# Performance work log

Measured on AMD Instinct MI355X. Metric: run time of the kernel, lower is better.

Reference implementation:

```python
import jax, jax.numpy as jnp
import numpy as np

DIM = 512      # model dim
HEADS = 8      # attention heads
WS = 256       # window_size
G = 32         # num_global_tokens
SPARSITY = 0.3 # fraction of entries masked out per row by the sparsity controller


def setup_inputs() -> dict:
    key = jax.random.key(0)
    ks = jax.random.split(key, 7)
    b, n = 4, 8192
    x = jax.random.normal(ks[0], (b, n, DIM), dtype=jnp.float32)
    w_qkv = jax.random.normal(ks[1], (DIM, 3 * DIM), dtype=jnp.float32) * (DIM ** -0.5)
    w_out = jax.random.normal(ks[2], (DIM, DIM), dtype=jnp.float32) * (DIM ** -0.5)
    b_out = jnp.zeros((DIM,), dtype=jnp.float32)
    local_bias = jax.random.normal(ks[3], (HEADS, WS, WS), dtype=jnp.float32)
    global_param = jax.random.normal(ks[4], (HEADS, G, WS), dtype=jnp.float32)
    gate = jax.random.normal(ks[5], (HEADS,), dtype=jnp.float32)
    return {"x": x, "w_qkv": w_qkv, "w_out": w_out, "b_out": b_out,
            "local_bias": local_bias, "global_param": global_param, "gate": gate}


def reference(x, w_qkv, w_out, b_out, local_bias, global_param, gate):
    b, n, _ = x.shape
    h, ws, g = HEADS, WS, G
    d = DIM // h
    w = n // ws  # number of windows
    scale = DIM ** -0.5

    qkv = x @ w_qkv                      # [b, n, 3*dim]
    q, k, v = jnp.split(qkv, 3, axis=-1)

    def to_win(t):  # [b, n, dim] -> [b, h, w, ws, d]
        return t.reshape(b, n, h, d).transpose(0, 2, 1, 3).reshape(b, h, w, ws, d)

    q, k, v = to_win(q), to_win(k), to_win(v)

    # windowed local attention with learned per-window additive bias
    local = jnp.einsum('bhwnd,bhwmd->bhwnm', q, k) * scale   # [b,h,w,ws,ws]
    local = local + local_bias[None, :, None]                # bias broadcast over b, w

    # global-token attention term built from window-averaged q/k
    q_mean = q.mean(axis=2)  # [b,h,ws,d]
    k_mean = k.mean(axis=2)  # [b,h,ws,d]
    global_q = jnp.einsum('hgn,bhnd->bhgd', global_param, q_mean)      # [b,h,g,d]
    global_scores = jnp.einsum('bhgd,bhmd->bhgm', global_q, k_mean) * scale  # [b,h,g,ws]
    global_bias = global_scores.mean(axis=2)                            # [b,h,ws]

    # sparsity controller: learned per-head gate combines local + global,
    # then top-k row sparsification keeps (1-sparsity) of entries pre-softmax
    gate_h = jax.nn.sigmoid(gate)[None, :, None, None, None]
    scores = local + gate_h * global_bias[:, :, None, None, :]          # [b,h,w,ws,ws]
    k_keep = int(ws * (1.0 - SPARSITY))
    thresh = jax.lax.top_k(scores, k_keep)[0][..., -1:]                 # kth largest per row
    scores = jnp.where(scores >= thresh, scores, jnp.float32(-1e9))

    attn = jax.nn.softmax(scores, axis=-1)
    out = jnp.einsum('bhwnm,bhwmd->bhwnd', attn, v)                     # [b,h,w,ws,d]
    out = out.reshape(b, h, n, d).transpose(0, 2, 1, 3).reshape(b, n, DIM)
    return out @ w_out + b_out
```

## Files before the change

### kernel.cpp

```cpp
#include <hip/hip_runtime.h>

#define NN    8192
#define WSZ   256
#define KKEEP 179
#define SCALE 0.044194173824159216f

typedef __attribute__((ext_vector_type(8))) __bf16 bf16x8;
typedef __attribute__((ext_vector_type(4))) short  s16x4;
typedef __attribute__((ext_vector_type(8))) short  s16x8;
typedef __attribute__((ext_vector_type(4))) float  f32x4;

struct Split3 { short h, m, l; };
__device__ __forceinline__ Split3 split3(float x)
{
    unsigned u  = __float_as_uint(x);
    unsigned hb = ((u + 0x7FFFu + ((u >> 16) & 1u)) >> 16) << 16;
    float r = x - __uint_as_float(hb);
    unsigned ur = __float_as_uint(r);
    unsigned mb = ((ur + 0x7FFFu + ((ur >> 16) & 1u)) >> 16) << 16;
    float r2 = r - __uint_as_float(mb);
    unsigned lr = __float_as_uint(r2);
    unsigned lb = (lr + 0x7FFFu + ((lr >> 16) & 1u)) >> 16;
    Split3 s;
    s.h = (short)(hb >> 16);
    s.m = (short)(mb >> 16);
    s.l = (short)(lb & 0xFFFFu);
    return s;
}

__device__ __forceinline__ void split2(float x, short& h, short& m)
{
    unsigned u  = __float_as_uint(x);
    unsigned hb = ((u + 0x7FFFu + ((u >> 16) & 1u)) >> 16) << 16;
    float r = x - __uint_as_float(hb);
    unsigned ur = __float_as_uint(r);
    unsigned mb = (ur + 0x7FFFu + ((ur >> 16) & 1u)) >> 16;
    h = (short)(hb >> 16);
    m = (short)(mb & 0xFFFFu);
}

__global__ __launch_bounds__(256) void splitw_kernel(const float* __restrict__ W,
                                                     int K, int N,
                                                     short* __restrict__ h,
                                                     short* __restrict__ m,
                                                     short* __restrict__ l)
{
    int idx = blockIdx.x * 256 + threadIdx.x;
    if (idx >= K * N) return;
    int k = idx / N, n = idx - k * N;
    Split3 s = split3(W[idx]);
    size_t o = (size_t)n * K + k;
    h[o] = s.h; m[o] = s.m; l[o] = s.l;
}

__global__ __launch_bounds__(256, 2) void gemm_mfma(const float* __restrict__ A, int lda,
                                                    const short* __restrict__ BTh,
                                                    const short* __restrict__ BTm,
                                                    const short* __restrict__ BTl,
                                                    const float* __restrict__ bias,
                                                    float* __restrict__ C, int ldc,
                                                    int qk_cols)
{
    __shared__ __align__(16) short Asm[3][128 * 40];
    __shared__ __align__(16) short Bsm[3][128 * 40];

    const int t       = threadIdx.x;
    const int lane    = t & 63;
    const int wave    = t >> 6;
    const int wr      = wave >> 1;
    const int wc      = wave & 1;
    const int rowBase = blockIdx.y * 128;
    const int colBase = blockIdx.x * 128;
    const int pstart  = (colBase < qk_cols) ? 0 : 3;

    const int sa[6] = {2, 0, 1, 1, 0, 0};
    const int sb[6] = {0, 2, 1, 0, 1, 0};

    const int fn = lane & 15;
    const int fq = (lane >> 4) * 8;

    f32x4 acc[4][4] = {};

    for (int ks = 0; ks < 512; ks += 32) {
        __syncthreads();

#pragma unroll
        for (int lo = 0; lo < 4; ++lo) {
            int idx = lo * 256 + t;
            int am  = idx >> 3;
            int af  = (idx & 7) * 4;
            float4 a4 = *(const float4*)&A[(size_t)(rowBase + am) * lda + ks + af];
            Split3 s0 = split3(a4.x);
            Split3 s1 = split3(a4.y);
            Split3 s2 = split3(a4.z);
            Split3 s3 = split3(a4.w);
            s16x4 hv, mv, lv;
            hv[0] = s0.h; hv[1] = s1.h; hv[2] = s2.h; hv[3] = s3.h;
            mv[0] = s0.m; mv[1] = s1.m; mv[2] = s2.m; mv[3] = s3.m;
            lv[0] = s0.l; lv[1] = s1.l; lv[2] = s2.l; lv[3] = s3.l;
            int o = am * 40 + af;
            *(s16x4*)&Asm[0][o] = hv;
            *(s16x4*)&Asm[1][o] = mv;
            *(s16x4*)&Asm[2][o] = lv;
        }
#pragma unroll
        for (int lo = 0; lo < 2; ++lo) {
            int c = lo * 256 + t;
            int n = c >> 2;
            int q = (c & 3) * 8;
            size_t src = (size_t)(colBase + n) * 512 + ks + q;
            int o = n * 40 + q;
            *(s16x8*)&Bsm[0][o] = *(const s16x8*)&BTh[src];
            *(s16x8*)&Bsm[1][o] = *(const s16x8*)&BTm[src];
            *(s16x8*)&Bsm[2][o] = *(const s16x8*)&BTl[src];
        }
        __syncthreads();

        bf16x8 Bf[3][4];
#pragma unroll
        for (int s = 0; s < 3; ++s)
#pragma unroll
            for (int j = 0; j < 4; ++j)
                Bf[s][j] = *(const bf16x8*)&Bsm[s][(wc * 64 + j * 16 + fn) * 40 + fq];

#pragma unroll
        for (int i = 0; i < 4; ++i) {
            bf16x8 Af[3];
#pragma unroll
            for (int s = 0; s < 3; ++s)
                Af[s] = *(const bf16x8*)&Asm[s][(wr * 64 + i * 16 + fn) * 40 + fq];
#pragma unroll
            for (int p = 0; p < 6; ++p) {
                if (p < pstart) continue;
#pragma unroll
                for (int j = 0; j < 4; ++j)
                    acc[i][j] = __builtin_amdgcn_mfma_f32_16x16x32_bf16(
                        Af[sa[p]], Bf[sb[p]][j], acc[i][j], 0, 0, 0);
            }
        }
    }

    const int crow0 = rowBase + wr * 64 + (lane >> 4) * 4;
    const int ccol0 = colBase + wc * 64 + fn;
#pragma unroll
    for (int j = 0; j < 4; ++j) {
        int col = ccol0 + j * 16;
        float bv = bias ? bias[col] : 0.0f;
#pragma unroll
        for (int i = 0; i < 4; ++i)
#pragma unroll
            for (int r = 0; r < 4; ++r)
                C[(size_t)(crow0 + i * 16 + r) * ldc + col] = acc[i][j][r] + bv;
    }
}

__global__ __launch_bounds__(256) void means_kernel(const float* __restrict__ qkv,
                                                    float* __restrict__ q_mean,
                                                    float* __restrict__ k_mean)
{
    int idx = blockIdx.x * 256 + threadIdx.x;
    int dd = idx & 63;
    int i  = (idx >> 6) & 255;
    int bh = idx >> 14;
    int b = bh >> 3, h = bh & 7;
    const float* base = qkv + (size_t)b * NN * 1536 + (size_t)h * 64 + dd;
    float qs = 0.f, ks = 0.f;
#pragma unroll
    for (int w = 0; w < 32; ++w) {
        size_t off = (size_t)(w * 256 + i) * 1536;
        qs += base[off];
        ks += base[off + 512];
    }
    q_mean[idx] = qs * 0.03125f;
    k_mean[idx] = ks * 0.03125f;
}

__global__ __launch_bounds__(256) void globalbias_kernel(const float* __restrict__ q_mean,
                                                         const float* __restrict__ k_mean,
                                                         const float* __restrict__ gp,
                                                         float* __restrict__ gbias)
{
    __shared__ float gq[32 * 64];
    const int bh = blockIdx.x;
    const int h  = bh & 7;
    const int t  = threadIdx.x;

#pragma unroll
    for (int e = 0; e < 8; ++e) {
        int idx = e * 256 + t;
        int g  = idx >> 6;
        int dd = idx & 63;
        const float* gpr = gp + (size_t)(h * 32 + g) * 256;
        const float* qm  = q_mean + (size_t)bh * 16384 + dd;
        float s = 0.f;
        for (int i = 0; i < 256; ++i) s += gpr[i] * qm[(size_t)i * 64];
        gq[idx] = s;
    }
    __syncthreads();

    const float* km = k_mean + (size_t)bh * 16384 + (size_t)t * 64;
    float4 kr[16];
#pragma unroll
    for (int j = 0; j < 16; ++j) kr[j] = *(const float4*)&km[4 * j];
    float acc = 0.f;
    for (int g = 0; g < 32; ++g) {
        const float* gqr = &gq[g * 64];
        float s = 0.f;
#pragma unroll
        for (int j = 0; j < 16; ++j) {
            float4 q4 = *(const float4*)&gqr[4 * j];
            s += q4.x * kr[j].x + q4.y * kr[j].y + q4.z * kr[j].z + q4.w * kr[j].w;
        }
        acc += s;
    }
    gbias[bh * 256 + t] = acc * SCALE * 0.03125f;
}

__device__ __forceinline__ unsigned mono_enc(float f) {
    unsigned u = __float_as_uint(f);
    return (u & 0x80000000u) ? ~u : (u | 0x80000000u);
}
__device__ __forceinline__ float mono_dec(unsigned e) {
    return (e & 0x80000000u) ? __uint_as_float(e ^ 0x80000000u)
                             : __uint_as_float(~e);
}

__global__ __launch_bounds__(256, 3) void attn_kernel(float* __restrict__ qkv,
                                                      const float* __restrict__ local_bias,
                                                      const float* __restrict__ gbias,
                                                      const float* __restrict__ gate)
{
    __shared__ __align__(16) short Qs[3 * 64 * 64];
    __shared__ __align__(16) short Ks[3 * 64 * 64];
    float* st = (float*)(void*)Ks;

    const int t    = threadIdx.x;
    const int lane = t & 63;
    const int wave = t >> 6;
    const int wr   = wave >> 1;
    const int wc   = wave & 1;
    const int fn   = lane & 15;
    const int fq   = (lane >> 4) * 8;
    const int g4   = (lane >> 4) * 4;

    const int blk = blockIdx.x;
    const int rc  = blk & 3;
    const int w   = (blk >> 2) & 31;
    const int bh  = blk >> 7;
    const int h   = bh & 7;
    const int b   = bh >> 3;
    const float gateh = 1.0f / (1.0f + __expf(-gate[h]));

    const size_t tokBase = (size_t)b * NN + (size_t)w * WSZ;
    float* qb = qkv + tokBase * 1536 + h * 64;
    const float* kb = qb + 512;
    const float* vb = qb + 1024;

    const int rr = t >> 2, sub = t & 3;

    const int sa[6] = {2, 0, 1, 1, 0, 0};
    const int sb[6] = {0, 2, 1, 0, 1, 0};

#pragma unroll
    for (int l = 0; l < 4; ++l) {
        int f  = l * 256 + t;
        int r  = f >> 4;
        int dg = (f & 15) * 4;
        float4 a4 = *(const float4*)&qb[(size_t)(rc * 64 + r) * 1536 + dg];
        Split3 s0 = split3(a4.x), s1 = split3(a4.y), s2 = split3(a4.z), s3 = split3(a4.w);
        s16x4 hv, mv, lv;
        hv[0] = s0.h; hv[1] = s1.h; hv[2] = s2.h; hv[3] = s3.h;
        mv[0] = s0.m; mv[1] = s1.m; mv[2] = s2.m; mv[3] = s3.m;
        lv[0] = s0.l; lv[1] = s1.l; lv[2] = s2.l; lv[3] = s3.l;
        int o = r * 64 + (dg ^ ((r & 7) << 3));
        *(s16x4*)&Qs[o]        = hv;
        *(s16x4*)&Qs[4096 + o] = mv;
        *(s16x4*)&Qs[8192 + o] = lv;
    }

    float vals[64];
#pragma unroll
    for (int mc = 0; mc < 4; ++mc) {
        __syncthreads();
#pragma unroll
        for (int l = 0; l < 4; ++l) {
            int f  = l * 256 + t;
            int m  = f >> 4;
            int dg = (f & 15) * 4;
            float4 a4 = *(const float4*)&kb[(size_t)(mc * 64 + m) * 1536 + dg];
            Split3 s0 = split3(a4.x), s1 = split3(a4.y), s2 = split3(a4.z), s3 = split3(a4.w);
            s16x4 hv, mv, lv;
            hv[0] = s0.h; hv[1] = s1.h; hv[2] = s2.h; hv[3] = s3.h;
            mv[0] = s0.m; mv[1] = s1.m; mv[2] = s2.m; mv[3] = s3.m;
            lv[0] = s0.l; lv[1] = s1.l; lv[2] = s2.l; lv[3] = s3.l;
            int o = m * 64 + (dg ^ ((m & 7) << 3));
            *(s16x4*)&Ks[o]        = hv;
            *(s16x4*)&Ks[4096 + o] = mv;
            *(s16x4*)&Ks[8192 + o] = lv;
        }
        __syncthreads();

        f32x4 acc[2][2] = {};
#pragma unroll
        for (int kk = 0; kk < 2; ++kk) {
            bf16x8 Af[3][2], Bf[3][2];
#pragma unroll
            for (int s = 0; s < 3; ++s)
#pragma unroll
                for (int i = 0; i < 2; ++i) {
                    int ar = wr * 32 + i * 16 + fn;
                    int bc = wc * 32 + i * 16 + fn;
                    Af[s][i] = *(const bf16x8*)&Qs[s * 4096 + ar * 64 + ((kk * 32 + fq) ^ ((ar & 7) << 3))];
                    Bf[s][i] = *(const bf16x8*)&Ks[s * 4096 + bc * 64 + ((kk * 32 + fq) ^ ((bc & 7) << 3))];
                }
#pragma unroll
            for (int p = 0; p < 6; ++p)
#pragma unroll
                for (int i = 0; i < 2; ++i)
#pragma unroll
                    for (int j = 0; j < 2; ++j)
                        acc[i][j] = __builtin_amdgcn_mfma_f32_16x16x32_bf16(
                            Af[sa[p]][i], Bf[sb[p]][j], acc[i][j], 0, 0, 0);
        }
        __syncthreads();

#pragma unroll
        for (int j = 0; j < 2; ++j) {
            int cl = wc * 32 + j * 16 + fn;
            int cf = mc * 64 + cl;
            float gb = gateh * gbias[bh * 256 + cf];
#pragma unroll
            for (int i = 0; i < 2; ++i)
#pragma unroll
                for (int r = 0; r < 4; ++r) {
                    int rl = wr * 32 + i * 16 + g4 + r;
                    st[rl * 68 + cl] = acc[i][j][r] * SCALE
                        + local_bias[((size_t)h * 256 + rc * 64 + rl) * 256 + cf] + gb;
                }
        }
        __syncthreads();
#pragma unroll
        for (int j = 0; j < 16; ++j)
            vals[mc * 16 + j] = st[rr * 68 + sub + 4 * j];
    }

    float rmin = vals[0], rmax = vals[0];
#pragma unroll
    for (int j = 1; j < 64; ++j) {
        rmin = fminf(rmin, vals[j]);
        rmax = fmaxf(rmax, vals[j]);
    }
    rmin = fminf(rmin, __shfl_xor(rmin, 1)); rmin = fminf(rmin, __shfl_xor(rmin, 2));
    rmax = fmaxf(rmax, __shfl_xor(rmax, 1)); rmax = fmaxf(rmax, __shfl_xor(rmax, 2));

    float flo = rmin, fhi = rmax;
    float thr = 0.f;
    bool  done = false;
    for (int it = 0; it < 16; ++it) {
        if (__all(done ? 1 : 0)) break;
        float mf = 0.5f * (flo + fhi);
        int c = 0;
#pragma unroll
        for (int j = 0; j < 64; ++j) c += (vals[j] >= mf) ? 1 : 0;
        c += __shfl_xor(c, 1);
        c += __shfl_xor(c, 2);
        if (!done) {
            if (c == KKEEP)      { thr = mf; done = true; }
            else if (c > KKEEP)  flo = mf;
            else                 fhi = mf;
        }
    }
    if (__any(done ? 0 : 1)) {
        unsigned lo_u = mono_enc(flo), hi_u = mono_enc(fhi);
        for (int it = 0; it < 34; ++it) {
            bool active = (!done) && (lo_u < hi_u);
            if (!__any(active ? 1 : 0)) break;
            unsigned span = hi_u - lo_u;
            unsigned mid  = lo_u + (span >> 1) + (span & 1u);
            float mf = mono_dec(mid);
            int c = 0;
#pragma unroll
            for (int j = 0; j < 64; ++j) c += (vals[j] >= mf) ? 1 : 0;
            c += __shfl_xor(c, 1);
            c += __shfl_xor(c, 2);
            if (active) {
                if (c == KKEEP)      { thr = mf; done = true; }
                else if (c >= KKEEP) lo_u = mid;
                else                 hi_u = mid - 1;
            }
        }
        if (!done) thr = mono_dec(lo_u);
    }

    float rmx = -3e38f;
#pragma unroll
    for (int j = 0; j < 64; ++j) rmx = fmaxf(rmx, (vals[j] >= thr) ? vals[j] : -3e38f);
    rmx = fmaxf(rmx, __shfl_xor(rmx, 1));
    rmx = fmaxf(rmx, __shfl_xor(rmx, 2));
    float rsum = 0.f;
#pragma unroll
    for (int j = 0; j < 64; ++j) {
        float e = (vals[j] >= thr) ? __expf(vals[j] - rmx) : 0.f;
        vals[j] = e;
        rsum += e;
    }
    rsum += __shfl_xor(rsum, 1);
    rsum += __shfl_xor(rsum, 2);
    float rinv = 1.0f / rsum;
#pragma unroll
    for (int j = 0; j < 64; ++j) vals[j] *= rinv;

    const int sa2[3] = {1, 0, 0};
    const int sb2[3] = {0, 1, 0};
    f32x4 acc2[2][2] = {};
#pragma unroll
    for (int mc = 0; mc < 4; ++mc) {
        __syncthreads();
#pragma unroll
        for (int u = 0; u < 16; ++u) {
            short ph, pm;
            split2(vals[mc * 16 + u], ph, pm);
            int ml   = sub + 4 * u;
            int slot = rr * 64 + (ml ^ ((rr & 7) << 3));
            Qs[slot]        = ph;
            Qs[4096 + slot] = pm;
        }
#pragma unroll
        for (int l = 0; l < 2; ++l) {
            int f  = l * 256 + t;
            int d  = f & 63;
            int mo = (f >> 6) * 8;
            s16x8 hv, mv;
#pragma unroll
            for (int i = 0; i < 8; ++i) {
                short vh, vm;
                split2(vb[(size_t)(mc * 64 + mo + i) * 1536 + d], vh, vm);
                hv[i] = vh; mv[i] = vm;
            }
            int o = d * 72 + mo;
            *(s16x8*)&Ks[o]        = hv;
            *(s16x8*)&Ks[4608 + o] = mv;
        }
        __syncthreads();

#pragma unroll
        for (int kk = 0; kk < 2; ++kk) {
            bf16x8 Pf[2][2], Vf[2][2];
#pragma unroll
            for (int s = 0; s < 2; ++s)
#pragma unroll
                for (int i = 0; i < 2; ++i) {
                    int pr = wr * 32 + i * 16 + fn;
                    int dr = wc * 32 + i * 16 + fn;
                    Pf[s][i] = *(const bf16x8*)&Qs[s * 4096 + pr * 64 + ((kk * 32 + fq) ^ ((pr & 7) << 3))];
                    Vf[s][i] = *(const bf16x8*)&Ks[s * 4608 + dr * 72 + kk * 32 + fq];
                }
#pragma unroll
            for (int p = 0; p < 3; ++p)
#pragma unroll
                for (int i = 0; i < 2; ++i)
#pragma unroll
                    for (int j = 0; j < 2; ++j)
                        acc2[i][j] = __builtin_amdgcn_mfma_f32_16x16x32_bf16(
                            Pf[sa2[p]][i], Vf[sb2[p]][j], acc2[i][j], 0, 0, 0);
        }
    }

#pragma unroll
    for (int j = 0; j < 2; ++j)
#pragma unroll
        for (int i = 0; i < 2; ++i)
#pragma unroll
            for (int r = 0; r < 4; ++r) {
                int row = rc * 64 + wr * 32 + i * 16 + g4 + r;
                int d   = wc * 32 + j * 16 + fn;
                qb[(size_t)row * 1536 + d] = acc2[i][j][r];
            }
}

extern "C" void kernel_launch(void* const* d_in, const int* in_sizes, int n_in,
                              void* d_out, int out_size, void* d_ws, size_t ws_size,
                              hipStream_t stream)
{
    (void)in_sizes; (void)n_in; (void)out_size; (void)ws_size;
    const float* x            = (const float*)d_in[0];
    const float* w_qkv        = (const float*)d_in[1];
    const float* w_out        = (const float*)d_in[2];
    const float* b_out        = (const float*)d_in[3];
    const float* local_bias   = (const float*)d_in[4];
    const float* global_param = (const float*)d_in[5];
    const float* gate         = (const float*)d_in[6];
    float* out = (float*)d_out;
    float* ws  = (float*)d_ws;

    float* qkv    = ws;
    float* q_mean = qkv + (size_t)32768 * 1536;
    float* k_mean = q_mean + (size_t)32 * 256 * 64;
    float* gb     = k_mean + (size_t)32 * 256 * 64;
    short* wsp    = (short*)(gb + 8192);
    short* WTh  = wsp;
    short* WTm  = WTh + (size_t)1536 * 512;
    short* WTl  = WTm + (size_t)1536 * 512;
    short* WoTh = WTl + (size_t)1536 * 512;
    short* WoTm = WoTh + (size_t)512 * 512;
    short* WoTl = WoTm + (size_t)512 * 512;

    splitw_kernel<<<3072, 256, 0, stream>>>(w_qkv, 512, 1536, WTh, WTm, WTl);
    splitw_kernel<<<1024, 256, 0, stream>>>(w_out, 512, 512, WoTh, WoTm, WoTl);
    gemm_mfma<<<dim3(12, 256), 256, 0, stream>>>(x, 512, WTh, WTm, WTl,
                                                 nullptr, qkv, 1536, 1024);
    means_kernel<<<2048, 256, 0, stream>>>(qkv, q_mean, k_mean);
    globalbias_kernel<<<32, 256, 0, stream>>>(q_mean, k_mean, global_param, gb);
    attn_kernel<<<4096, 256, 0, stream>>>(qkv, local_bias, gb, gate);
    gemm_mfma<<<dim3(4, 256), 256, 0, stream>>>(qkv, 1536, WoTh, WoTm, WoTl,
                                                b_out, out, 512, 0);
}
```

Measured before the change: 740.3 us.

## Retune split-bf16 GEMM: swizzled LDS, XCD remap, truncating split, 2-term V path

```diff
diff --git a/kernel.cpp b/kernel.cpp
--- a/kernel.cpp
+++ b/kernel.cpp
@@ -5,6 +5,9 @@
 #define KKEEP 179
 #define SCALE 0.044194173824159216f
 
+#define BPLANE  ((size_t)1536 * 512)
+#define OPLANE  ((size_t)512 * 512)
+
 typedef __attribute__((ext_vector_type(8))) __bf16 bf16x8;
 typedef __attribute__((ext_vector_type(4))) short  s16x4;
 typedef __attribute__((ext_vector_type(8))) short  s16x8;
@@ -14,36 +17,39 @@
 __device__ __forceinline__ Split3 split3(float x)
 {
     unsigned u  = __float_as_uint(x);
-    unsigned hb = ((u + 0x7FFFu + ((u >> 16) & 1u)) >> 16) << 16;
-    float r = x - __uint_as_float(hb);
+    float hf = __uint_as_float(u & 0xFFFF0000u);
+    float r  = x - hf;
     unsigned ur = __float_as_uint(r);
-    unsigned mb = ((ur + 0x7FFFu + ((ur >> 16) & 1u)) >> 16) << 16;
-    float r2 = r - __uint_as_float(mb);
+    float mf = __uint_as_float(ur & 0xFFFF0000u);
+    float r2 = r - mf;
     unsigned lr = __float_as_uint(r2);
     unsigned lb = (lr + 0x7FFFu + ((lr >> 16) & 1u)) >> 16;
     Split3 s;
-    s.h = (short)(hb >> 16);
-    s.m = (short)(mb >> 16);
+    s.h = (short)(u >> 16);
+    s.m = (short)(ur >> 16);
     s.l = (short)(lb & 0xFFFFu);
     return s;
 }
 
-__device__ __forceinline__ void split2(float x, short& h, short& m)
+struct Split2 { short h, m; };
+__device__ __forceinline__ Split2 split2(float x)
 {
     unsigned u  = __float_as_uint(x);
     unsigned hb = ((u + 0x7FFFu + ((u >> 16) & 1u)) >> 16) << 16;
     float r = x - __uint_as_float(hb);
     unsigned ur = __float_as_uint(r);
     unsigned mb = (ur + 0x7FFFu + ((ur >> 16) & 1u)) >> 16;
-    h = (short)(hb >> 16);
-    m = (short)(mb & 0xFFFFu);
-}
-
-__global__ __launch_bounds__(256) void splitw_kernel(const float* __restrict__ W,
-                                                     int K, int N,
-                                                     short* __restrict__ h,
-                                                     short* __restrict__ m,
-                                                     short* __restrict__ l)
+    Split2 s;
+    s.h = (short)(hb >> 16);
+    s.m = (short)(mb & 0xFFFFu);
+    return s;
+}
+
+__global__ __launch_bounds__(256) void splitw3_kernel(const float* __restrict__ W,
+                                                      int K, int N,
+                                                      short* __restrict__ h,
+                                                      short* __restrict__ m,
+                                                      short* __restrict__ l)
 {
     int idx = blockIdx.x * 256 + threadIdx.x;
     if (idx >= K * N) return;
@@ -53,7 +59,20 @@
     h[o] = s.h; m[o] = s.m; l[o] = s.l;
 }
 
-__global__ __launch_bounds__(256, 2) void gemm_mfma(const float* __restrict__ A, int lda,
+__global__ __launch_bounds__(256) void splitw2_kernel(const float* __restrict__ W,
+                                                      int K, int N,
+                                                      short* __restrict__ h,
+                                                      short* __restrict__ m)
+{
+    int idx = blockIdx.x * 256 + threadIdx.x;
+    if (idx >= K * N) return;
+    int k = idx / N, n = idx - k * N;
+    Split2 s = split2(W[idx]);
+    size_t o = (size_t)n * K + k;
+    h[o] = s.h; m[o] = s.m;
+}
+
+__global__ __launch_bounds__(256, 3) void gemm_mfma(const float* __restrict__ A, int lda,
                                                     const short* __restrict__ BTh,
                                                     const short* __restrict__ BTm,
                                                     const short* __restrict__ BTl,
@@ -61,23 +80,25 @@
                                                     float* __restrict__ C, int ldc,
                                                     int qk_cols)
 {
-    __shared__ __align__(16) short Asm[3][128 * 40];
-    __shared__ __align__(16) short Bsm[3][128 * 40];
-
-    const int t       = threadIdx.x;
-    const int lane    = t & 63;
-    const int wave    = t >> 6;
-    const int wr      = wave >> 1;
-    const int wc      = wave & 1;
-    const int rowBase = blockIdx.y * 128;
-    const int colBase = blockIdx.x * 128;
-    const int pstart  = (colBase < qk_cols) ? 0 : 3;
-
-    const int sa[6] = {2, 0, 1, 1, 0, 0};
-    const int sb[6] = {0, 2, 1, 0, 1, 0};
-
-    const int fn = lane & 15;
-    const int fq = (lane >> 4) * 8;
+    __shared__ __align__(16) short Asm[3][128 * 32];
+    __shared__ __align__(16) short Bsm[3][128 * 32];
+
+    const int t    = threadIdx.x;
+    const int lane = t & 63;
+    const int wave = t >> 6;
+    const int wr   = wave >> 1;
+    const int wc   = wave & 1;
+
+    const int nwg = gridDim.x * gridDim.y;
+    const int lin = blockIdx.x + gridDim.x * blockIdx.y;
+    const int cpx = nwg >> 3;
+    const int w2  = (lin & 7) * cpx + (lin >> 3);
+    const int rowBase = (w2 / gridDim.x) * 128;
+    const int colBase = (w2 % gridDim.x) * 128;
+    const bool full   = (colBase < qk_cols);
+
+    const int fn   = lane & 15;
+    const int slot = lane >> 4;
 
     f32x4 acc[4][4] = {};
 
@@ -90,18 +111,30 @@
             int am  = idx >> 3;
             int af  = (idx & 7) * 4;
             float4 a4 = *(const float4*)&A[(size_t)(rowBase + am) * lda + ks + af];
-            Split3 s0 = split3(a4.x);
-            Split3 s1 = split3(a4.y);
-            Split3 s2 = split3(a4.z);
-            Split3 s3 = split3(a4.w);
-            s16x4 hv, mv, lv;
-            hv[0] = s0.h; hv[1] = s1.h; hv[2] = s2.h; hv[3] = s3.h;
-            mv[0] = s0.m; mv[1] = s1.m; mv[2] = s2.m; mv[3] = s3.m;
-            lv[0] = s0.l; lv[1] = s1.l; lv[2] = s2.l; lv[3] = s3.l;
-            int o = am * 40 + af;
-            *(s16x4*)&Asm[0][o] = hv;
-            *(s16x4*)&Asm[1][o] = mv;
-            *(s16x4*)&Asm[2][o] = lv;
+            int o = am * 32 + (((af >> 3) ^ ((am >> 1) & 3)) << 3) + (af & 4);
+            if (full) {
+                Split3 s0 = split3(a4.x);
+                Split3 s1 = split3(a4.y);
+                Split3 s2 = split3(a4.z);
+                Split3 s3 = split3(a4.w);
+                s16x4 hv, mv, lv;
+                hv[0] = s0.h; hv[1] = s1.h; hv[2] = s2.h; hv[3] = s3.h;
+                mv[0] = s0.m; mv[1] = s1.m; mv[2] = s2.m; mv[3] = s3.m;
+                lv[0] = s0.l; lv[1] = s1.l; lv[2] = s2.l; lv[3] = s3.l;
+                *(s16x4*)&Asm[0][o] = hv;
+                *(s16x4*)&Asm[1][o] = mv;
+                *(s16x4*)&Asm[2][o] = lv;
+            } else {
+                Split2 s0 = split2(a4.x);
+                Split2 s1 = split2(a4.y);
+                Split2 s2 = split2(a4.z);
+                Split2 s3 = split2(a4.w);
+                s16x4 hv, mv;
+                hv[0] = s0.h; hv[1] = s1.h; hv[2] = s2.h; hv[3] = s3.h;
+                mv[0] = s0.m; mv[1] = s1.m; mv[2] = s2.m; mv[3] = s3.m;
+                *(s16x4*)&Asm[0][o] = hv;
+                *(s16x4*)&Asm[1][o] = mv;
+            }
         }
 #pragma unroll
         for (int lo = 0; lo < 2; ++lo) {
@@ -109,33 +142,53 @@
             int n = c >> 2;
             int q = (c & 3) * 8;
             size_t src = (size_t)(colBase + n) * 512 + ks + q;
-            int o = n * 40 + q;
+            int o = n * 32 + (((q >> 3) ^ ((n >> 1) & 3)) << 3);
             *(s16x8*)&Bsm[0][o] = *(const s16x8*)&BTh[src];
             *(s16x8*)&Bsm[1][o] = *(const s16x8*)&BTm[src];
-            *(s16x8*)&Bsm[2][o] = *(const s16x8*)&BTl[src];
+            if (full) *(s16x8*)&Bsm[2][o] = *(const s16x8*)&BTl[src];
         }
         __syncthreads();
 
         bf16x8 Bf[3][4];
 #pragma unroll
-        for (int s = 0; s < 3; ++s)
-#pragma unroll
-            for (int j = 0; j < 4; ++j)
-                Bf[s][j] = *(const bf16x8*)&Bsm[s][(wc * 64 + j * 16 + fn) * 40 + fq];
+        for (int s = 0; s < 2; ++s)
+#pragma unroll
+            for (int j = 0; j < 4; ++j) {
+                int rowb = wc * 64 + j * 16 + fn;
+                Bf[s][j] = *(const bf16x8*)&Bsm[s][rowb * 32
+                                                   + ((slot ^ ((rowb >> 1) & 3)) << 3)];
+            }
+        if (full)
+#pragma unroll
+            for (int j = 0; j < 4; ++j) {
+                int rowb = wc * 64 + j * 16 + fn;
+                Bf[2][j] = *(const bf16x8*)&Bsm[2][rowb * 32
+                                                   + ((slot ^ ((rowb >> 1) & 3)) << 3)];
+            }
 
 #pragma unroll
         for (int i = 0; i < 4; ++i) {
-            bf16x8 Af[3];
-#pragma unroll
-            for (int s = 0; s < 3; ++s)
-                Af[s] = *(const bf16x8*)&Asm[s][(wr * 64 + i * 16 + fn) * 40 + fq];
-#pragma unroll
-            for (int p = 0; p < 6; ++p) {
-                if (p < pstart) continue;
-#pragma unroll
-                for (int j = 0; j < 4; ++j)
-                    acc[i][j] = __builtin_amdgcn_mfma_f32_16x16x32_bf16(
-                        Af[sa[p]], Bf[sb[p]][j], acc[i][j], 0, 0, 0);
+            int rowa = wr * 64 + i * 16 + fn;
+            bf16x8 Ah = *(const bf16x8*)&Asm[0][rowa * 32 + ((slot ^ ((rowa >> 1) & 3)) << 3)];
+            bf16x8 Am = *(const bf16x8*)&Asm[1][rowa * 32 + ((slot ^ ((rowa >> 1) & 3)) << 3)];
+            if (full) {
+                bf16x8 Al = *(const bf16x8*)&Asm[2][rowa * 32 + ((slot ^ ((rowa >> 1) & 3)) << 3)];
+#pragma unroll
+                for (int j = 0; j < 4; ++j) {
+                    acc[i][j] = __builtin_amdgcn_mfma_f32_16x16x32_bf16(Al, Bf[0][j], acc[i][j], 0, 0, 0);
+                    acc[i][j] = __builtin_amdgcn_mfma_f32_16x16x32_bf16(Ah, Bf[2][j], acc[i][j], 0, 0, 0);
+                    acc[i][j] = __builtin_amdgcn_mfma_f32_16x16x32_bf16(Am, Bf[1][j], acc[i][j], 0, 0, 0);
+                    acc[i][j] = __builtin_amdgcn_mfma_f32_16x16x32_bf16(Am, Bf[0][j], acc[i][j], 0, 0, 0);
+                    acc[i][j] = __builtin_amdgcn_mfma_f32_16x16x32_bf16(Ah, Bf[1][j], acc[i][j], 0, 0, 0);
+                    acc[i][j] = __builtin_amdgcn_mfma_f32_16x16x32_bf16(Ah, Bf[0][j], acc[i][j], 0, 0, 0);
+                }
+            } else {
+#pragma unroll
+                for (int j = 0; j < 4; ++j) {
+                    acc[i][j] = __builtin_amdgcn_mfma_f32_16x16x32_bf16(Am, Bf[0][j], acc[i][j], 0, 0, 0);
+                    acc[i][j] = __builtin_amdgcn_mfma_f32_16x16x32_bf16(Ah, Bf[1][j], acc[i][j], 0, 0, 0);
+                    acc[i][j] = __builtin_amdgcn_mfma_f32_16x16x32_bf16(Ah, Bf[0][j], acc[i][j], 0, 0, 0);
+                }
             }
         }
     }
@@ -243,7 +296,8 @@
     const int fq   = (lane >> 4) * 8;
     const int g4   = (lane >> 4) * 4;
 
-    const int blk = blockIdx.x;
+    const int bid = blockIdx.x;
+    const int blk = ((bid & 7) << 9) | (bid >> 3);
     const int rc  = blk & 3;
     const int w   = (blk >> 2) & 31;
     const int bh  = blk >> 7;
@@ -353,25 +407,10 @@
     rmin = fminf(rmin, __shfl_xor(rmin, 1)); rmin = fminf(rmin, __shfl_xor(rmin, 2));
     rmax = fmaxf(rmax, __shfl_xor(rmax, 1)); rmax = fmaxf(rmax, __shfl_xor(rmax, 2));
 
-    float flo = rmin, fhi = rmax;
-    float thr = 0.f;
+    float thr = rmin;
     bool  done = false;
-    for (int it = 0; it < 16; ++it) {
-        if (__all(done ? 1 : 0)) break;
-        float mf = 0.5f * (flo + fhi);
-        int c = 0;
-#pragma unroll
-        for (int j = 0; j < 64; ++j) c += (vals[j] >= mf) ? 1 : 0;
-        c += __shfl_xor(c, 1);
-        c += __shfl_xor(c, 2);
-        if (!done) {
-            if (c == KKEEP)      { thr = mf; done = true; }
-            else if (c > KKEEP)  flo = mf;
-            else                 fhi = mf;
-        }
-    }
-    if (__any(done ? 0 : 1)) {
-        unsigned lo_u = mono_enc(flo), hi_u = mono_enc(fhi);
+    {
+        unsigned lo_u = mono_enc(rmin), hi_u = mono_enc(rmax);
         for (int it = 0; it < 34; ++it) {
             bool active = (!done) && (lo_u < hi_u);
             if (!__any(active ? 1 : 0)) break;
@@ -418,12 +457,11 @@
         __syncthreads();
 #pragma unroll
         for (int u = 0; u < 16; ++u) {
-            short ph, pm;
-            split2(vals[mc * 16 + u], ph, pm);
-            int ml   = sub + 4 * u;
-            int slot = rr * 64 + (ml ^ ((rr & 7) << 3));
-            Qs[slot]        = ph;
-            Qs[4096 + slot] = pm;
+            Split2 sp = split2(vals[mc * 16 + u]);
+            int ml     = sub + 4 * u;
+            int pslot  = rr * 64 + (ml ^ ((rr & 7) << 3));
+            Qs[pslot]        = sp.h;
+            Qs[4096 + pslot] = sp.m;
         }
 #pragma unroll
         for (int l = 0; l < 2; ++l) {
@@ -433,9 +471,8 @@
             s16x8 hv, mv;
 #pragma unroll
             for (int i = 0; i < 8; ++i) {
-                short vh, vm;
-                split2(vb[(size_t)(mc * 64 + mo + i) * 1536 + d], vh, vm);
-                hv[i] = vh; mv[i] = vm;
+                Split2 sp = split2(vb[(size_t)(mc * 64 + mo + i) * 1536 + d]);
+                hv[i] = sp.h; mv[i] = sp.m;
             }
             int o = d * 72 + mo;
             *(s16x8*)&Ks[o]        = hv;
@@ -497,21 +534,19 @@
     float* q_mean = qkv + (size_t)32768 * 1536;
     float* k_mean = q_mean + (size_t)32 * 256 * 64;
     float* gb     = k_mean + (size_t)32 * 256 * 64;
-    short* wsp    = (short*)(gb + 8192);
-    short* WTh  = wsp;
-    short* WTm  = WTh + (size_t)1536 * 512;
-    short* WTl  = WTm + (size_t)1536 * 512;
-    short* WoTh = WTl + (size_t)1536 * 512;
-    short* WoTm = WoTh + (size_t)512 * 512;
-    short* WoTl = WoTm + (size_t)512 * 512;
-
-    splitw_kernel<<<3072, 256, 0, stream>>>(w_qkv, 512, 1536, WTh, WTm, WTl);
-    splitw_kernel<<<1024, 256, 0, stream>>>(w_out, 512, 512, WoTh, WoTm, WoTl);
-    gemm_mfma<<<dim3(12, 256), 256, 0, stream>>>(x, 512, WTh, WTm, WTl,
+    short* WoB    = (short*)(gb + 8192);
+    short* WqB    = WoB + 2 * OPLANE;
+
+    splitw2_kernel<<<1024, 256, 0, stream>>>(w_out, 512, 512, WoB, WoB + OPLANE);
+    splitw3_kernel<<<3072, 256, 0, stream>>>(w_qkv, 512, 1536,
+                                             WqB, WqB + BPLANE, WqB + 2 * BPLANE);
+    gemm_mfma<<<dim3(12, 256), 256, 0, stream>>>(x, 512, WqB, WqB + BPLANE,
+                                                 WqB + 2 * BPLANE,
                                                  nullptr, qkv, 1536, 1024);
     means_kernel<<<2048, 256, 0, stream>>>(qkv, q_mean, k_mean);
     globalbias_kernel<<<32, 256, 0, stream>>>(q_mean, k_mean, global_param, gb);
     attn_kernel<<<4096, 256, 0, stream>>>(qkv, local_bias, gb, gate);
-    gemm_mfma<<<dim3(4, 256), 256, 0, stream>>>(qkv, 1536, WoTh, WoTm, WoTl,
+    gemm_mfma<<<dim3(4, 256), 256, 0, stream>>>(qkv, 1536, WoB, WoB + OPLANE,
+                                                WoB,
                                                 b_out, out, 512, 0);
 }
```

Result: slower. 1.228 ms (+65.9%).
